# Optimization experiments

Measured on AMD Instinct MI355X. Metric: run time of the kernel, lower is better.

## Reference

```python
import jax, jax.numpy as jnp
import numpy as np

N_NODES = 50000
N_EDGES = 600000
D_EMB = 128
D_HID = 128
N_HEADS = 4
N_MABS = 7  # ISAB0(mab0,mab1), ISAB1(mab0,mab1), PMA, SAB, SAB
B, S = 16, 512
PROTO = 5


def setup_inputs() -> dict:
    key = jax.random.key(0)
    ks = jax.random.split(key, 24)
    nrm = lambda k, shape, s=0.05: jax.random.normal(k, shape, jnp.float32) * s
    node_embed = nrm(ks[0], (N_NODES + 1, D_EMB), 1.0).at[0].set(0.0)  # padding_idx=0
    return {
        'node_ids': jax.random.randint(ks[1], (B, S), 0, N_NODES),
        'edge_idx': jax.random.randint(ks[2], (2, N_EDGES), 0, N_NODES),
        'edge_attr': jax.random.normal(ks[3], (N_EDGES,), jnp.float32),
        'node_embed': node_embed,
        'lin_W': nrm(ks[4], (D_EMB, D_HID)), 'lin_b': jnp.zeros((D_HID,), jnp.float32),
        'gat_W': nrm(ks[5], (D_HID, D_HID)),
        'gat_att_src': nrm(ks[6], (D_HID,)), 'gat_att_dst': nrm(ks[7], (D_HID,)),
        'gat_bias': jnp.zeros((D_HID,), jnp.float32),
        'mab_Wq': nrm(ks[8], (N_MABS, D_HID, D_HID)), 'mab_bq': jnp.zeros((N_MABS, D_HID), jnp.float32),
        'mab_Wk': nrm(ks[9], (N_MABS, D_HID, D_HID)), 'mab_bk': jnp.zeros((N_MABS, D_HID), jnp.float32),
        'mab_Wv': nrm(ks[10], (N_MABS, D_HID, D_HID)), 'mab_bv': jnp.zeros((N_MABS, D_HID), jnp.float32),
        'mab_Wo': nrm(ks[11], (N_MABS, D_HID, D_HID)), 'mab_bo': jnp.zeros((N_MABS, D_HID), jnp.float32),
        'isab_I': nrm(ks[12], (2, 1, D_HID), 1.0),   # 2 ISAB blocks, num_inds=1
        'pma_S': nrm(ks[13], (1, D_HID), 1.0),       # num_outputs=1 seed
        'dec_W': nrm(ks[14], (D_HID, D_HID)), 'dec_b': jnp.zeros((D_HID,), jnp.float32),
        'prototypes': nrm(ks[15], (1, PROTO, D_HID), 1.0),
    }


def mab(Q, K, Wq, bq, Wk, bk, Wv, bv, Wo, bo):
    # Set-transformer MAB, ln=False; residual uses projected Q; scale by sqrt(full dim)
    D = Q.shape[-1]
    h, d = N_HEADS, D // N_HEADS
    Qp = Q @ Wq + bq
    Kp = K @ Wk + bk
    Vp = K @ Wv + bv
    sh = lambda x: x.reshape(x.shape[0], x.shape[1], h, d).transpose(0, 2, 1, 3)
    A = jax.nn.softmax(jnp.einsum('bhqd,bhkd->bhqk', sh(Qp), sh(Kp)) / np.sqrt(D).astype(np.float32))
    O = sh(Qp) + jnp.einsum('bhqk,bhkd->bhqd', A, sh(Vp))
    O = O.transpose(0, 2, 1, 3).reshape(Q.shape[0], Q.shape[1], D)
    return O + jax.nn.relu(O @ Wo + bo)


def reference(node_ids, edge_idx, edge_attr, node_embed, lin_W, lin_b, gat_W,
              gat_att_src, gat_att_dst, gat_bias, mab_Wq, mab_bq, mab_Wk, mab_bk,
              mab_Wv, mab_bv, mab_Wo, mab_bo, isab_I, pma_S, dec_W, dec_b, prototypes):
    # embed all nodes then linear
    x = node_embed[jnp.arange(N_NODES)] @ lin_W + lin_b          # [N, H]
    # GATConv (1 head, negative_slope=0.2, add_self_loops=True; edge_attr unused)
    loops = jnp.arange(N_NODES)
    src = jnp.concatenate([edge_idx[0], loops])
    dst = jnp.concatenate([edge_idx[1], loops])
    xw = x @ gat_W                                               # [N, H]
    a_s = xw @ gat_att_src                                       # [N]
    a_d = xw @ gat_att_dst
    e = jax.nn.leaky_relu(a_s[src] + a_d[dst], 0.2)              # [E+N]
    m = jax.ops.segment_max(e, dst, num_segments=N_NODES)
    ex = jnp.exp(e - m[dst])
    den = jax.ops.segment_sum(ex, dst, num_segments=N_NODES)
    coef = ex / den[dst]
    x = jax.ops.segment_sum(coef[:, None] * xw[src], dst, num_segments=N_NODES) + gat_bias
    # gather per-sample node sets
    X = x[node_ids]                                              # [B, S, H]
    b = X.shape[0]
    def mb(i, Q, K):
        return mab(Q, K, mab_Wq[i], mab_bq[i], mab_Wk[i], mab_bk[i],
                   mab_Wv[i], mab_bv[i], mab_Wo[i], mab_bo[i])
    # encoder: 2 ISAB blocks (num_inds=1)
    for i in range(2):
        Hb = mb(2 * i, jnp.broadcast_to(isab_I[i][None], (b, 1, D_HID)), X)
        X = mb(2 * i + 1, X, Hb)
    # decoder: PMA -> SAB -> SAB -> Linear
    X = mb(4, jnp.broadcast_to(pma_S[None], (b, 1, D_HID)), X)
    X = mb(5, X, X)
    X = mb(6, X, X)
    X = X @ dec_W + dec_b                                        # [B, 1, H]
    proto = jnp.broadcast_to(prototypes, (b, PROTO, D_HID))
    return jnp.concatenate([X, proto], axis=1)                   # [B, 6, H]
```

## Files before the change

kernel.cpp:

```cpp
#include <hip/hip_runtime.h>
#include <math.h>

#define N_NODES 50000
#define N_EDGES 600000
#define BATCH 16
#define SEQ 512
#define NROWS (BATCH*SEQ)
#define N_ITEMS (N_EDGES + N_NODES)

#define OFF_X      0L
#define OFF_ACC    1048576L
#define OFF_X2     2097152L
#define OFF_AS     3145728L
#define OFF_AD     3195728L
#define OFF_WC     3245728L
#define OFF_BC     3262112L
#define OFF_QP     3262240L
#define OFF_WKH    3262624L
#define OFF_CKH    3264160L
#define OFF_VAS    3264176L
#define OFF_VAD    3264304L
#define OFF_BFIN   3264432L
#define OFF_CSD    3264560L
#define OFF_VPOD   3264564L
#define OFF_UP     3266612L
#define OFF_SP     3332148L
#define OFF_PWH    3332660L
#define OFF_PWL    3373620L
#define OFF_MASK   3414580L
#define OFF_DEG    (OFF_MASK + 50000L)
#define OFF_FILL   (OFF_DEG + 8192L)
#define OFF_CNT    (OFF_FILL + 8192L)
#define ZERO_BYTES ((50000L + 8192L + 8192L + 4L) * 4L)
#define OFF_MAP    (OFF_CNT + 4L)
#define OFF_INV    (OFF_MAP + 50000L)
#define OFF_ROWPTR (OFF_INV + 8192L)
#define OFF_COL    (OFF_ROWPTR + 8194L)

typedef __attribute__((ext_vector_type(8))) short bf16x8;
typedef __attribute__((ext_vector_type(4))) float f32x4;
#define MFMA16(a,b,c) __builtin_amdgcn_mfma_f32_16x16x32_bf16(a,b,c,0,0,0)

__device__ __forceinline__ unsigned short f2bf_rne(float f) {
    unsigned int u = __float_as_uint(f);
    unsigned int r = u + 0x7FFFu + ((u >> 16) & 1u);
    return (unsigned short)(r >> 16);
}
__device__ __forceinline__ float bf2f(unsigned short h) {
    return __uint_as_float(((unsigned int)h) << 16);
}

__global__ __launch_bounds__(256) void prep_kernel(
    const float* __restrict__ lin_W, const float* __restrict__ lin_b,
    const float* __restrict__ gat_W,
    const float* __restrict__ mab_Wq, const float* __restrict__ mab_bq,
    const float* __restrict__ isab_I, const float* __restrict__ pma_S,
    float* __restrict__ Wc, float* __restrict__ bc, float* __restrict__ qp)
{
    int t = blockIdx.x * 256 + threadIdx.x;
    if (t < 16384) {
        int i = t >> 7, j = t & 127;
        float s = 0.f;
        for (int k = 0; k < 128; ++k) s += lin_W[i*128 + k] * gat_W[k*128 + j];
        Wc[t] = s;
    } else if (t < 16512) {
        int j = t - 16384;
        float s = 0.f;
        for (int k = 0; k < 128; ++k) s += lin_b[k] * gat_W[k*128 + j];
        bc[j] = s;
    } else if (t < 16896) {
        int u = t - 16512;
        int m = u >> 7, c = u & 127;
        int mi = m * 2;
        const float* vec = (m == 0) ? isab_I : (m == 1 ? isab_I + 128 : pma_S);
        float s = mab_bq[mi*128 + c];
        for (int k = 0; k < 128; ++k) s += vec[k] * mab_Wq[mi*16384 + k*128 + c];
        qp[u] = s;
    }
}

__global__ __launch_bounds__(256) void pack2_kernel(
    const float* __restrict__ Wc, const float* __restrict__ bc,
    const float* __restrict__ qp,
    const float* __restrict__ mab_Wq, const float* __restrict__ mab_Wo,
    const float* __restrict__ mab_Wk, const float* __restrict__ mab_bk,
    const float* __restrict__ att_src, const float* __restrict__ att_dst,
    const float* __restrict__ gat_bias,
    unsigned short* __restrict__ pWh, unsigned short* __restrict__ pWl,
    float* __restrict__ wkh, float* __restrict__ ckh,
    float* __restrict__ vas, float* __restrict__ vad,
    float* __restrict__ bfin, float* __restrict__ csd)
{
    int b = blockIdx.x, t = threadIdx.x;
    if (b < 320) {
        int tid = b*256 + t;
        int m = tid >> 14;
        int e = tid & 16383;
        int j = e & 7, l = (e>>3) & 63, ct = (e>>9) & 7, kc = e >> 12;
        int k = kc*32 + (l>>4)*8 + j;
        int c = ct*16 + (l & 15);
        const float* src;
        if (m == 0) src = Wc;
        else if (m == 1) src = mab_Wq + 1*16384;
        else if (m == 2) src = mab_Wo + 1*16384;
        else if (m == 3) src = mab_Wq + 3*16384;
        else src = mab_Wo + 3*16384;
        float v = src[k*128 + c];
        unsigned short h = f2bf_rne(v);
        pWh[tid] = h;
        pWl[tid] = f2bf_rne(v - bf2f(h));
    } else if (b == 320) {
        for (int it = 0; it < 6; ++it) {
            int u = it*256 + t;
            int m = u >> 9, h = (u >> 7) & 3, j = u & 127;
            const float* Wk = mab_Wk + (2*m)*16384 + j*128 + h*32;
            const float* q  = qp + m*128 + h*32;
            float s = 0.f;
            #pragma unroll
            for (int d = 0; d < 32; ++d) s += Wk[d] * q[d];
            wkh[u] = s;
        }
        if (t < 12) {
            int m = t >> 2, h = t & 3;
            const float* bk = mab_bk + (2*m)*128 + h*32;
            const float* q  = qp + m*128 + h*32;
            float s = 0.f;
            #pragma unroll
            for (int d = 0; d < 32; ++d) s += bk[d] * q[d];
            ckh[t] = s;
        }
    } else {
        if (t < 128) {
            float s = 0.f;
            for (int j = 0; j < 128; ++j) s += Wc[t*128 + j] * att_src[j];
            vas[t] = s;
            bfin[t] = bc[t] + gat_bias[t];
        } else {
            int k = t - 128;
            float s = 0.f;
            for (int j = 0; j < 128; ++j) s += Wc[k*128 + j] * att_dst[j];
            vad[k] = s;
        }
        if (t == 0) {
            float s = 0.f;
            for (int j = 0; j < 128; ++j) s += bc[j] * att_src[j];
            csd[0] = s;
        }
        if (t == 1) {
            float s = 0.f;
            for (int j = 0; j < 128; ++j) s += bc[j] * att_dst[j];
            csd[1] = s;
        }
    }
}

__device__ __forceinline__ void mfma_stage(
    const float (*Xs)[132], int arow, int ao, int lane,
    const unsigned short* __restrict__ pWh, const unsigned short* __restrict__ pWl,
    f32x4 acc[8])
{
    #pragma unroll
    for (int kc = 0; kc < 4; ++kc) {
        float4 fa = *(const float4*)&Xs[arow][kc*32 + ao];
        float4 fb = *(const float4*)&Xs[arow][kc*32 + ao + 4];
        float f[8] = {fa.x, fa.y, fa.z, fa.w, fb.x, fb.y, fb.z, fb.w};
        bf16x8 ah, al;
        #pragma unroll
        for (int j = 0; j < 8; ++j) {
            unsigned short h = f2bf_rne(f[j]);
            ah[j] = (short)h;
            al[j] = (short)f2bf_rne(f[j] - bf2f(h));
        }
        #pragma unroll
        for (int ct = 0; ct < 8; ++ct) {
            int fo = ((kc*8 + ct)*64 + lane)*8;
            bf16x8 bh = *(const bf16x8*)(pWh + fo);
            bf16x8 bl = *(const bf16x8*)(pWl + fo);
            acc[ct] = MFMA16(ah, bh, acc[ct]);
            acc[ct] = MFMA16(ah, bl, acc[ct]);
            acc[ct] = MFMA16(al, bh, acc[ct]);
        }
    }
}

__global__ __launch_bounds__(256) void mfma_lin_kernel(
    const float* __restrict__ Xin,
    const unsigned short* __restrict__ pWh, const unsigned short* __restrict__ pWl,
    const float* __restrict__ b1, float* __restrict__ out)
{
    __shared__ float Xs[64][132];
    int t = threadIdx.x;
    long row0 = (long)blockIdx.x * 64;
    #pragma unroll
    for (int i = 0; i < 32; ++i) {
        int idx = i*256 + t;
        int r = idx >> 7, k = idx & 127;
        Xs[r][k] = Xin[(row0 + r)*128 + k];
    }
    __syncthreads();
    int lane = t & 63, wv = t >> 6;
    int arow = wv*16 + (lane & 15), ao = (lane >> 4)*8;
    int crow0 = wv*16 + (lane >> 4)*4, ccol = lane & 15;
    f32x4 acc[8];
    #pragma unroll
    for (int ct = 0; ct < 8; ++ct) { acc[ct][0]=0.f; acc[ct][1]=0.f; acc[ct][2]=0.f; acc[ct][3]=0.f; }
    mfma_stage(Xs, arow, ao, lane, pWh, pWl, acc);
    #pragma unroll
    for (int ct = 0; ct < 8; ++ct) {
        int cc = ct*16 + ccol;
        float bb = b1[cc];
        #pragma unroll
        for (int i = 0; i < 4; ++i)
            out[(row0 + crow0 + i)*128 + cc] = acc[ct][i] + bb;
    }
}

__global__ __launch_bounds__(256) void mfma_odd_kernel(
    const float* __restrict__ Xin,
    const unsigned short* __restrict__ pQh, const unsigned short* __restrict__ pQl,
    const float* __restrict__ bq, const float* __restrict__ vpod,
    const unsigned short* __restrict__ pOh, const unsigned short* __restrict__ pOl,
    const float* __restrict__ bo, float* __restrict__ Xout)
{
    __shared__ float Xs[64][132];
    int t = threadIdx.x;
    long row0 = (long)blockIdx.x * 64;
    #pragma unroll
    for (int i = 0; i < 32; ++i) {
        int idx = i*256 + t;
        int r = idx >> 7, k = idx & 127;
        Xs[r][k] = Xin[(row0 + r)*128 + k];
    }
    __syncthreads();
    int lane = t & 63, wv = t >> 6;
    int arow = wv*16 + (lane & 15), ao = (lane >> 4)*8;
    int crow0 = wv*16 + (lane >> 4)*4, ccol = lane & 15;
    int bidx = (int)(row0 >> 9);
    f32x4 acc[8];
    #pragma unroll
    for (int ct = 0; ct < 8; ++ct) { acc[ct][0]=0.f; acc[ct][1]=0.f; acc[ct][2]=0.f; acc[ct][3]=0.f; }
    mfma_stage(Xs, arow, ao, lane, pQh, pQl, acc);
    #pragma unroll
    for (int ct = 0; ct < 8; ++ct) {
        int cc = ct*16 + ccol;
        float bb = bq[cc] + vpod[bidx*128 + cc];
        #pragma unroll
        for (int i = 0; i < 4; ++i) Xs[crow0 + i][cc] = acc[ct][i] + bb;
    }
    #pragma unroll
    for (int ct = 0; ct < 8; ++ct) { acc[ct][0]=0.f; acc[ct][1]=0.f; acc[ct][2]=0.f; acc[ct][3]=0.f; }
    mfma_stage(Xs, arow, ao, lane, pOh, pOl, acc);
    #pragma unroll
    for (int ct = 0; ct < 8; ++ct) {
        int cc = ct*16 + ccol;
        float bb = bo[cc];
        #pragma unroll
        for (int i = 0; i < 4; ++i) {
            float o1 = Xs[crow0 + i][cc];
            Xout[(row0 + crow0 + i)*128 + cc] = o1 + fmaxf(acc[ct][i] + bb, 0.f);
        }
    }
}

__global__ __launch_bounds__(256) void avec_kernel(
    const float* __restrict__ embed, const float* __restrict__ vas,
    const float* __restrict__ vad, const float* __restrict__ csd,
    const int* __restrict__ node_ids, int* __restrict__ mask,
    float* __restrict__ a_s, float* __restrict__ a_d)
{
    if (blockIdx.x < 32) {
        int idx = blockIdx.x*256 + threadIdx.x;
        mask[node_ids[idx]] = 1;
    }
    int w = threadIdx.x >> 6, lane = threadIdx.x & 63;
    long row = (long)blockIdx.x * 4 + w;
    const float* xr = embed + row*128 + lane*2;
    float x0 = xr[0], x1 = xr[1];
    float s = x0*vas[lane*2] + x1*vas[lane*2 + 1];
    float d = x0*vad[lane*2] + x1*vad[lane*2 + 1];
    #pragma unroll
    for (int off = 32; off > 0; off >>= 1) {
        s += __shfl_down(s, off);
        d += __shfl_down(d, off);
    }
    if (lane == 0) { a_s[row] = s + csd[0]; a_d[row] = d + csd[1]; }
}

__global__ __launch_bounds__(256) void assign_kernel(
    const int* __restrict__ mask, int* __restrict__ map,
    int* __restrict__ inv, int* __restrict__ counter)
{
    __shared__ int wbase[4];
    int i = blockIdx.x*256 + threadIdx.x;
    bool act = (i < N_NODES) && mask[i];
    unsigned long long m = __ballot(act);
    int lane = threadIdx.x & 63;
    int w = threadIdx.x >> 6;
    if (lane == 0) wbase[w] = __popcll(m);
    __syncthreads();
    if (threadIdx.x == 0) {
        int tot = wbase[0] + wbase[1] + wbase[2] + wbase[3];
        int base = atomicAdd(counter, tot);
        int r = base;
        #pragma unroll
        for (int j = 0; j < 4; ++j) { int cj = wbase[j]; wbase[j] = r; r += cj; }
    }
    __syncthreads();
    if (i < N_NODES) {
        int c = -1;
        if (act) {
            c = wbase[w] + __popcll(m & ((1ull << lane) - 1ull));
            inv[c] = i;
        }
        map[i] = c;
    }
}

__global__ __launch_bounds__(256) void pass1_kernel(
    const int* __restrict__ edge_idx, const int* __restrict__ map,
    int* __restrict__ deg)
{
    int i = blockIdx.x*256 + threadIdx.x;
    if (i >= N_ITEMS) return;
    int dd = (i < N_EDGES) ? edge_idx[N_EDGES + i] : i - N_EDGES;
    int c = map[dd];
    if (c >= 0) atomicAdd(&deg[c], 1);
}

__global__ __launch_bounds__(256) void scan_kernel(const int* __restrict__ deg,
                                                   int* __restrict__ rowptr)
{
    __shared__ int part[256];
    __shared__ int pref[256];
    int t = threadIdx.x;
    int base = t * 32;
    int s = 0;
    #pragma unroll
    for (int j = 0; j < 32; ++j) s += deg[base + j];
    part[t] = s;
    __syncthreads();
    if (t == 0) {
        int run = 0;
        for (int i = 0; i < 256; ++i) { pref[i] = run; run += part[i]; }
    }
    __syncthreads();
    int run = pref[t];
    #pragma unroll
    for (int j = 0; j < 32; ++j) { rowptr[base + j] = run; run += deg[base + j]; }
    if (t == 255) rowptr[8192] = run;
}

__global__ __launch_bounds__(256) void pass2_kernel(
    const int* __restrict__ edge_idx, const int* __restrict__ map,
    const int* __restrict__ rowptr, int* __restrict__ fill,
    int* __restrict__ colx)
{
    int i = blockIdx.x*256 + threadIdx.x;
    if (i >= N_ITEMS) return;
    int s, dd;
    if (i < N_EDGES) { s = edge_idx[i]; dd = edge_idx[N_EDGES + i]; }
    else             { s = dd = i - N_EDGES; }
    int c = map[dd];
    if (c < 0) return;
    int pos = rowptr[c] + atomicAdd(&fill[c], 1);
    colx[pos] = s;
}

__global__ __launch_bounds__(256) void agg_kernel(
    const int* __restrict__ rowptr, const int* __restrict__ colx,
    const int* __restrict__ inv, const int* __restrict__ cnt,
    const float* __restrict__ a_s, const float* __restrict__ a_d,
    const float* __restrict__ embed, float* __restrict__ acc)
{
    int c = blockIdx.x*4 + (threadIdx.x >> 6);
    int lane = threadIdx.x & 63;
    if (c >= *cnt) return;
    int dd = inv[c];
    float ad = a_d[dd];
    int beg = rowptr[c], end = rowptr[c + 1];
    float s0 = 0.f, s1 = 0.f, den = 0.f;
    for (int j = beg; j < end; ++j) {
        int s = colx[j];
        float e = a_s[s] + ad;
        e = (e > 0.f) ? e : 0.2f * e;
        float ex = __expf(e);
        den += ex;
        float2 v = *(const float2*)(embed + (long)s*128 + lane*2);
        s0 += ex * v.x;
        s1 += ex * v.y;
    }
    float inv_d = 1.f / den;
    float* o = acc + (long)c*128 + lane*2;
    o[0] = s0 * inv_d;
    o[1] = s1 * inv_d;
}

__global__ __launch_bounds__(256) void gather_kernel(
    const int* __restrict__ node_ids, const int* __restrict__ map,
    const float* __restrict__ X2, float* __restrict__ X)
{
    int w = threadIdx.x >> 6, lane = threadIdx.x & 63;
    int j = blockIdx.x*4 + w;
    int c = map[node_ids[j]];
    const float2 v = *(const float2*)(X2 + (long)c*128 + lane*2);
    *(float2*)(X + (long)j*128 + lane*2) = v;
}

__global__ __launch_bounds__(256) void attn_partA_kernel(
    const float* __restrict__ X, const float* __restrict__ wkh,
    const float* __restrict__ ckh, float* __restrict__ up, float* __restrict__ sp)
{
    __shared__ float wks[4][128];
    __shared__ float esm[4][64];
    int b = blockIdx.x >> 3, chunk = blockIdx.x & 7;
    int t = threadIdx.x;
    #pragma unroll
    for (int i = 0; i < 2; ++i) {
        int u = i*256 + t;
        wks[u >> 7][u & 127] = wkh[u];
    }
    __syncthreads();
    const float scale = 0.088388347648318447f;
    int wv = t >> 6, lane = t & 63;
    {
        const float* xr = X + ((long)b*512 + chunk*64 + lane)*128;
        float l = 0.f;
        for (int d4 = 0; d4 < 128; d4 += 4) {
            float4 xv = *(const float4*)&xr[d4];
            l += xv.x*wks[wv][d4] + xv.y*wks[wv][d4+1]
               + xv.z*wks[wv][d4+2] + xv.w*wks[wv][d4+3];
        }
        float e = __expf((l + ckh[wv]) * scale);
        esm[wv][lane] = e;
        float s = e;
        #pragma unroll
        for (int off = 32; off > 0; off >>= 1) s += __shfl_down(s, off);
        if (lane == 0) sp[(b*8 + chunk)*4 + wv] = s;
    }
    __syncthreads();
    {
        int hh = t >> 7, d = t & 127;
        float a0 = 0.f, a1 = 0.f;
        const float* xc = X + ((long)b*512 + chunk*64)*128 + d;
        for (int k = 0; k < 64; ++k) {
            float xv = xc[(long)k*128];
            a0 += esm[2*hh][k] * xv;
            a1 += esm[2*hh + 1][k] * xv;
        }
        up[((b*8 + chunk)*4 + 2*hh)*128 + d] = a0;
        up[((b*8 + chunk)*4 + 2*hh + 1)*128 + d] = a1;
    }
}

__device__ __forceinline__ float matvec_qs(
    const float* __restrict__ W, const float* xs, float (*red)[128], int t)
{
    int c = t & 127, q = t >> 7;
    float acc = 0.f;
    #pragma unroll
    for (int j = 0; j < 32; ++j) {
        int k = q*32 + j;
        acc += xs[k] * W[k*128 + c];
    }
    red[q][c] = acc;
    __syncthreads();
    float s = 0.f;
    if (t < 128) s = red[0][t] + red[1][t] + red[2][t] + red[3][t];
    __syncthreads();
    return s;
}

__global__ __launch_bounds__(512) void attn_evenB_kernel(
    const float* __restrict__ up, const float* __restrict__ sp,
    const float* __restrict__ qp,
    const float* __restrict__ Wv, const float* __restrict__ bv,
    const float* __restrict__ Wo, const float* __restrict__ bo,
    const float* __restrict__ Wv1, const float* __restrict__ bv1,
    float* __restrict__ vpod)
{
    __shared__ float u_sm[4][128];
    __shared__ float red[4][128];
    __shared__ float qs[128], Ovec[128], Hsm[128];
    int b = blockIdx.x, t = threadIdx.x;
    {
        float s = Wv[t*32] + Wo[t*32] + Wv1[t*32];
        asm volatile("" :: "v"(s));
    }
    if (t < 128) qs[t] = qp[t];
    {
        int h = t >> 7, d = t & 127;
        float s = 0.f, dn = 0.f;
        #pragma unroll
        for (int c = 0; c < 8; ++c) {
            s  += up[((b*8 + c)*4 + h)*128 + d];
            dn += sp[(b*8 + c)*4 + h];
        }
        u_sm[h][d] = s / dn;
    }
    __syncthreads();
    {
        int q4 = t >> 7, c = t & 127, h = c >> 5;
        float a = 0.f;
        #pragma unroll
        for (int j = 0; j < 32; ++j) {
            int k = q4*32 + j;
            a += u_sm[h][k] * Wv[k*128 + c];
        }
        red[q4][c] = a;
    }
    __syncthreads();
    if (t < 128) Ovec[t] = qs[t] + red[0][t] + red[1][t] + red[2][t] + red[3][t] + bv[t];
    __syncthreads();
    float mv = matvec_qs(Wo, Ovec, red, t);
    if (t < 128) Hsm[t] = Ovec[t] + fmaxf(mv + bo[t], 0.f);
    __syncthreads();
    float mv2 = matvec_qs(Wv1, Hsm, red, t);
    if (t < 128) vpod[b*128 + t] = mv2 + bv1[t];
}

__global__ __launch_bounds__(512) void attn_pmaB_kernel(
    const float* __restrict__ up, const float* __restrict__ sp,
    const float* __restrict__ qp,
    const float* __restrict__ mab_Wq, const float* __restrict__ mab_bq,
    const float* __restrict__ mab_Wv, const float* __restrict__ mab_bv,
    const float* __restrict__ mab_Wo, const float* __restrict__ mab_bo,
    const float* __restrict__ dec_W, const float* __restrict__ dec_b,
    const float* __restrict__ protos, float* __restrict__ out)
{
    __shared__ float u_sm[4][128];
    __shared__ float red[4][128];
    __shared__ float qs[128], Ovec[128], S1[128], S2[128];
    int b = blockIdx.x, t = threadIdx.x;
    {
        const float* wq = mab_Wq + 5*16384;
        const float* wv = mab_Wv + 4*16384;
        const float* wo = mab_Wo + 4*16384;
        float s = 0.f;
        #pragma unroll
        for (int i = 0; i < 2; ++i) s += wq[(t + 512*i)*32];
        #pragma unroll
        for (int i = 0; i < 3; ++i) { s += wv[(t + 512*i)*32]; s += wo[(t + 512*i)*32]; }
        s += dec_W[t*32];
        asm volatile("" :: "v"(s));
    }
    if (t < 128) qs[t] = qp[t];
    {
        int h = t >> 7, d = t & 127;
        float s = 0.f, dn = 0.f;
        #pragma unroll
        for (int c = 0; c < 8; ++c) {
            s  += up[((b*8 + c)*4 + h)*128 + d];
            dn += sp[(b*8 + c)*4 + h];
        }
        u_sm[h][d] = s / dn;
    }
    __syncthreads();
    {
        int q4 = t >> 7, c = t & 127, h = c >> 5;
        float a = 0.f;
        #pragma unroll
        for (int j = 0; j < 32; ++j) {
            int k = q4*32 + j;
            a += u_sm[h][k] * (mab_Wv + 4*16384)[k*128 + c];
        }
        red[q4][c] = a;
    }
    __syncthreads();
    if (t < 128) Ovec[t] = qs[t] + red[0][t] + red[1][t] + red[2][t] + red[3][t]
                         + mab_bv[4*128 + t];
    __syncthreads();
    float mv = matvec_qs(mab_Wo + 4*16384, Ovec, red, t);
    if (t < 128) S1[t] = Ovec[t] + fmaxf(mv + mab_bo[4*128 + t], 0.f);
    __syncthreads();
    float q5 = matvec_qs(mab_Wq + 5*16384, S1, red, t);
    float v5 = matvec_qs(mab_Wv + 5*16384, S1, red, t);
    if (t < 128) S2[t] = q5 + mab_bq[5*128 + t] + v5 + mab_bv[5*128 + t];
    __syncthreads();
    float m5 = matvec_qs(mab_Wo + 5*16384, S2, red, t);
    if (t < 128) S1[t] = S2[t] + fmaxf(m5 + mab_bo[5*128 + t], 0.f);
    __syncthreads();
    float q6 = matvec_qs(mab_Wq + 6*16384, S1, red, t);
    float v6 = matvec_qs(mab_Wv + 6*16384, S1, red, t);
    if (t < 128) S2[t] = q6 + mab_bq[6*128 + t] + v6 + mab_bv[6*128 + t];
    __syncthreads();
    float m6 = matvec_qs(mab_Wo + 6*16384, S2, red, t);
    if (t < 128) S1[t] = S2[t] + fmaxf(m6 + mab_bo[6*128 + t], 0.f);
    __syncthreads();
    float y = matvec_qs(dec_W, S1, red, t);
    if (t < 128) out[b*768 + t] = y + dec_b[t];
    {
        int p = t >> 7, c = t & 127;
        out[b*768 + (1 + p)*128 + c] = protos[p*128 + c];
        if (t < 128) out[b*768 + 640 + t] = protos[512 + t];
    }
}

extern "C" void kernel_launch(void* const* d_in, const int* in_sizes, int n_in,
                              void* d_out, int out_size, void* d_ws, size_t ws_size,
                              hipStream_t stream)
{
    (void)in_sizes; (void)n_in; (void)out_size; (void)ws_size;
    const int*   node_ids  = (const int*)d_in[0];
    const int*   edge_idx  = (const int*)d_in[1];
    const float* node_embed= (const float*)d_in[3];
    const float* lin_W     = (const float*)d_in[4];
    const float* lin_b     = (const float*)d_in[5];
    const float* gat_W     = (const float*)d_in[6];
    const float* att_src   = (const float*)d_in[7];
    const float* att_dst   = (const float*)d_in[8];
    const float* gat_bias  = (const float*)d_in[9];
    const float* mab_Wq    = (const float*)d_in[10];
    const float* mab_bq    = (const float*)d_in[11];
    const float* mab_Wk    = (const float*)d_in[12];
    const float* mab_bk    = (const float*)d_in[13];
    const float* mab_Wv    = (const float*)d_in[14];
    const float* mab_bv    = (const float*)d_in[15];
    const float* mab_Wo    = (const float*)d_in[16];
    const float* mab_bo    = (const float*)d_in[17];
    const float* isab_I    = (const float*)d_in[18];
    const float* pma_S     = (const float*)d_in[19];
    const float* dec_W     = (const float*)d_in[20];
    const float* dec_b     = (const float*)d_in[21];
    const float* protos    = (const float*)d_in[22];

    float* ws    = (float*)d_ws;
    float* X     = ws + OFF_X;
    float* acc   = ws + OFF_ACC;
    float* X2    = ws + OFF_X2;
    float* a_s   = ws + OFF_AS;
    float* a_d   = ws + OFF_AD;
    float* Wc    = ws + OFF_WC;
    float* bc    = ws + OFF_BC;
    float* qp    = ws + OFF_QP;
    float* wkh   = ws + OFF_WKH;
    float* ckh   = ws + OFF_CKH;
    float* vas   = ws + OFF_VAS;
    float* vad   = ws + OFF_VAD;
    float* bfin  = ws + OFF_BFIN;
    float* csd   = ws + OFF_CSD;
    float* vpod  = ws + OFF_VPOD;
    float* up    = ws + OFF_UP;
    float* sp    = ws + OFF_SP;
    unsigned short* pWh = (unsigned short*)(ws + OFF_PWH);
    unsigned short* pWl = (unsigned short*)(ws + OFF_PWL);
    int*   mask  = (int*)(ws + OFF_MASK);
    int*   deg   = (int*)(ws + OFF_DEG);
    int*   fill  = (int*)(ws + OFF_FILL);
    int*   cnt   = (int*)(ws + OFF_CNT);
    int*   map   = (int*)(ws + OFF_MAP);
    int*   inv   = (int*)(ws + OFF_INV);
    int*   rowp  = (int*)(ws + OFF_ROWPTR);
    int*   colx  = (int*)(ws + OFF_COL);
    float* out   = (float*)d_out;

    hipMemsetAsync(ws + OFF_MASK, 0, ZERO_BYTES, stream);

    prep_kernel<<<66, 256, 0, stream>>>(lin_W, lin_b, gat_W, mab_Wq, mab_bq, isab_I, pma_S,
                                        Wc, bc, qp);
    pack2_kernel<<<322, 256, 0, stream>>>(Wc, bc, qp, mab_Wq, mab_Wo, mab_Wk, mab_bk,
                                          att_src, att_dst, gat_bias,
                                          pWh, pWl, wkh, ckh, vas, vad, bfin, csd);
    avec_kernel<<<N_NODES/4, 256, 0, stream>>>(node_embed, vas, vad, csd, node_ids, mask,
                                               a_s, a_d);
    assign_kernel<<<(N_NODES + 255)/256, 256, 0, stream>>>(mask, map, inv, cnt);
    pass1_kernel<<<(N_ITEMS + 255)/256, 256, 0, stream>>>(edge_idx, map, deg);
    scan_kernel<<<1, 256, 0, stream>>>(deg, rowp);
    pass2_kernel<<<(N_ITEMS + 255)/256, 256, 0, stream>>>(edge_idx, map, rowp, fill, colx);
    agg_kernel<<<NROWS/4, 256, 0, stream>>>(rowp, colx, inv, cnt, a_s, a_d, node_embed, acc);
    mfma_lin_kernel<<<NROWS/64, 256, 0, stream>>>(acc, pWh, pWl, bfin, X2);
    gather_kernel<<<NROWS/4, 256, 0, stream>>>(node_ids, map, X2, X);

    for (int i = 0; i < 2; ++i) {
        int o = 2*i + 1;
        attn_partA_kernel<<<128, 256, 0, stream>>>(X, wkh + i*512, ckh + i*4, up, sp);
        attn_evenB_kernel<<<16, 512, 0, stream>>>(up, sp, qp + i*128,
                                                  mab_Wv + (2*i)*16384, mab_bv + (2*i)*128,
                                                  mab_Wo + (2*i)*16384, mab_bo + (2*i)*128,
                                                  mab_Wv + o*16384, mab_bv + o*128,
                                                  vpod);
        int mq = 1 + 2*i;
        int mo = 2 + 2*i;
        mfma_odd_kernel<<<NROWS/64, 256, 0, stream>>>(X,
                                                      pWh + mq*16384, pWl + mq*16384,
                                                      mab_bq + o*128, vpod,
                                                      pWh + mo*16384, pWl + mo*16384,
                                                      mab_bo + o*128, X);
    }
    attn_partA_kernel<<<128, 256, 0, stream>>>(X, wkh + 1024, ckh + 8, up, sp);
    attn_pmaB_kernel<<<16, 512, 0, stream>>>(up, sp, qp + 256,
                                             mab_Wq, mab_bq, mab_Wv, mab_bv, mab_Wo, mab_bo,
                                             dec_W, dec_b, protos, out);
}
```

Before: 279.1 us.

## Fuse attention partA into gather and odd MAB kernels, drop avec pass

Removes the avec kernel, which computed per-node attention scalars for all 50000 nodes, and instead computes source/destination scores on the fly inside agg_kernel with wave reductions over the embedding rows it already loads. The node mask setup moves into extra blocks of pack2. The gather and attn_partA kernels are fused into gatherA, and partA is also fused into the tail of the odd MAB kernel, reusing the shared-memory tile instead of rereading X from global memory. The scan is rewritten with a wave-level shuffle prefix in place of a serial loop. The trade-off is a redundant per-edge dot product and reduction in agg, plus fewer launches and less global traffic.

```diff
diff --git a/kernel.cpp b/kernel.cpp
--- a/kernel.cpp
+++ b/kernel.cpp
@@ -11,8 +11,6 @@
 #define OFF_X      0L
 #define OFF_ACC    1048576L
 #define OFF_X2     2097152L
-#define OFF_AS     3145728L
-#define OFF_AD     3195728L
 #define OFF_WC     3245728L
 #define OFF_BC     3262112L
 #define OFF_QP     3262240L
@@ -49,6 +47,11 @@
 __device__ __forceinline__ float bf2f(unsigned short h) {
     return __uint_as_float(((unsigned int)h) << 16);
 }
+__device__ __forceinline__ float wave_allsum(float x) {
+    #pragma unroll
+    for (int off = 32; off > 0; off >>= 1) x += __shfl_xor(x, off);
+    return x;
+}
 
 __global__ __launch_bounds__(256) void prep_kernel(
     const float* __restrict__ lin_W, const float* __restrict__ lin_b,
@@ -85,11 +88,12 @@
     const float* __restrict__ mab_Wq, const float* __restrict__ mab_Wo,
     const float* __restrict__ mab_Wk, const float* __restrict__ mab_bk,
     const float* __restrict__ att_src, const float* __restrict__ att_dst,
-    const float* __restrict__ gat_bias,
+    const float* __restrict__ gat_bias, const int* __restrict__ node_ids,
     unsigned short* __restrict__ pWh, unsigned short* __restrict__ pWl,
     float* __restrict__ wkh, float* __restrict__ ckh,
     float* __restrict__ vas, float* __restrict__ vad,
-    float* __restrict__ bfin, float* __restrict__ csd)
+    float* __restrict__ bfin, float* __restrict__ csd,
+    int* __restrict__ mask)
 {
     int b = blockIdx.x, t = threadIdx.x;
     if (b < 320) {
@@ -129,7 +133,7 @@
             for (int d = 0; d < 32; ++d) s += bk[d] * q[d];
             ckh[t] = s;
         }
-    } else {
+    } else if (b == 321) {
         if (t < 128) {
             float s = 0.f;
             for (int j = 0; j < 128; ++j) s += Wc[t*128 + j] * att_src[j];
@@ -151,6 +155,9 @@
             for (int j = 0; j < 128; ++j) s += bc[j] * att_dst[j];
             csd[1] = s;
         }
+    } else {
+        int idx = (b - 322)*256 + t;
+        mask[node_ids[idx]] = 1;
     }
 }
 
@@ -183,6 +190,41 @@
     }
 }
 
+__device__ __forceinline__ void partA_phase(
+    const float (*Xs)[132], const float (*wks)[128], float (*esm)[64],
+    const float* __restrict__ ckh, int blk, int t,
+    float* __restrict__ up, float* __restrict__ sp)
+{
+    const float scale = 0.088388347648318447f;
+    int wv = t >> 6, lane = t & 63;
+    {
+        float l = 0.f;
+        for (int d4 = 0; d4 < 128; d4 += 4) {
+            float4 xv = *(const float4*)&Xs[lane][d4];
+            l += xv.x*wks[wv][d4] + xv.y*wks[wv][d4+1]
+               + xv.z*wks[wv][d4+2] + xv.w*wks[wv][d4+3];
+        }
+        float e = __expf((l + ckh[wv]) * scale);
+        esm[wv][lane] = e;
+        float s = e;
+        #pragma unroll
+        for (int off = 32; off > 0; off >>= 1) s += __shfl_down(s, off);
+        if (lane == 0) sp[blk*4 + wv] = s;
+    }
+    __syncthreads();
+    {
+        int hh = t >> 7, d = t & 127;
+        float a0 = 0.f, a1 = 0.f;
+        for (int k = 0; k < 64; ++k) {
+            float xv = Xs[k][d];
+            a0 += esm[2*hh][k] * xv;
+            a1 += esm[2*hh + 1][k] * xv;
+        }
+        up[(blk*4 + 2*hh)*128 + d] = a0;
+        up[(blk*4 + 2*hh + 1)*128 + d] = a1;
+    }
+}
+
 __global__ __launch_bounds__(256) void mfma_lin_kernel(
     const float* __restrict__ Xin,
     const unsigned short* __restrict__ pWh, const unsigned short* __restrict__ pWl,
@@ -215,22 +257,56 @@
     }
 }
 
-__global__ __launch_bounds__(256) void mfma_odd_kernel(
+__global__ __launch_bounds__(256) void gatherA_kernel(
+    const int* __restrict__ node_ids, const int* __restrict__ map,
+    const float* __restrict__ X2, const float* __restrict__ wkh,
+    const float* __restrict__ ckh,
+    float* __restrict__ X, float* __restrict__ up, float* __restrict__ sp)
+{
+    __shared__ float Xs[64][132];
+    __shared__ float wks[4][128];
+    __shared__ float esm[4][64];
+    __shared__ int cmap[64];
+    int blk = blockIdx.x, t = threadIdx.x;
+    long j0 = (long)blk * 64;
+    if (t < 64) cmap[t] = map[node_ids[j0 + t]];
+    #pragma unroll
+    for (int i = 0; i < 2; ++i) { int u = i*256 + t; wks[u >> 7][u & 127] = wkh[u]; }
+    __syncthreads();
+    #pragma unroll
+    for (int i = 0; i < 8; ++i) {
+        int idx = i*256 + t;
+        int r = idx >> 5, k4 = (idx & 31)*4;
+        float4 v = *(const float4*)(X2 + (long)cmap[r]*128 + k4);
+        *(float4*)&Xs[r][k4] = v;
+        *(float4*)(X + (j0 + r)*128 + k4) = v;
+    }
+    __syncthreads();
+    partA_phase(Xs, wks, esm, ckh, blk, t, up, sp);
+}
+
+__global__ __launch_bounds__(256) void odd_fused_kernel(
     const float* __restrict__ Xin,
     const unsigned short* __restrict__ pQh, const unsigned short* __restrict__ pQl,
     const float* __restrict__ bq, const float* __restrict__ vpod,
     const unsigned short* __restrict__ pOh, const unsigned short* __restrict__ pOl,
-    const float* __restrict__ bo, float* __restrict__ Xout)
+    const float* __restrict__ bo,
+    const float* __restrict__ wkh, const float* __restrict__ ckh,
+    float* __restrict__ Xout, float* __restrict__ up, float* __restrict__ sp)
 {
     __shared__ float Xs[64][132];
-    int t = threadIdx.x;
-    long row0 = (long)blockIdx.x * 64;
+    __shared__ float wks[4][128];
+    __shared__ float esm[4][64];
+    int blk = blockIdx.x, t = threadIdx.x;
+    long row0 = (long)blk * 64;
     #pragma unroll
     for (int i = 0; i < 32; ++i) {
         int idx = i*256 + t;
         int r = idx >> 7, k = idx & 127;
         Xs[r][k] = Xin[(row0 + r)*128 + k];
     }
+    #pragma unroll
+    for (int i = 0; i < 2; ++i) { int u = i*256 + t; wks[u >> 7][u & 127] = wkh[u]; }
     __syncthreads();
     int lane = t & 63, wv = t >> 6;
     int arow = wv*16 + (lane & 15), ao = (lane >> 4)*8;
@@ -257,33 +333,13 @@
         #pragma unroll
         for (int i = 0; i < 4; ++i) {
             float o1 = Xs[crow0 + i][cc];
-            Xout[(row0 + crow0 + i)*128 + cc] = o1 + fmaxf(acc[ct][i] + bb, 0.f);
-        }
-    }
-}
-
-__global__ __launch_bounds__(256) void avec_kernel(
-    const float* __restrict__ embed, const float* __restrict__ vas,
-    const float* __restrict__ vad, const float* __restrict__ csd,
-    const int* __restrict__ node_ids, int* __restrict__ mask,
-    float* __restrict__ a_s, float* __restrict__ a_d)
-{
-    if (blockIdx.x < 32) {
-        int idx = blockIdx.x*256 + threadIdx.x;
-        mask[node_ids[idx]] = 1;
-    }
-    int w = threadIdx.x >> 6, lane = threadIdx.x & 63;
-    long row = (long)blockIdx.x * 4 + w;
-    const float* xr = embed + row*128 + lane*2;
-    float x0 = xr[0], x1 = xr[1];
-    float s = x0*vas[lane*2] + x1*vas[lane*2 + 1];
-    float d = x0*vad[lane*2] + x1*vad[lane*2 + 1];
-    #pragma unroll
-    for (int off = 32; off > 0; off >>= 1) {
-        s += __shfl_down(s, off);
-        d += __shfl_down(d, off);
-    }
-    if (lane == 0) { a_s[row] = s + csd[0]; a_d[row] = d + csd[1]; }
+            float v = o1 + fmaxf(acc[ct][i] + bb, 0.f);
+            Xout[(row0 + crow0 + i)*128 + cc] = v;
+            Xs[crow0 + i][cc] = v;
+        }
+    }
+    __syncthreads();
+    partA_phase(Xs, wks, esm, ckh, blk, t, up, sp);
 }
 
 __global__ __launch_bounds__(256) void assign_kernel(
@@ -330,21 +386,24 @@
 __global__ __launch_bounds__(256) void scan_kernel(const int* __restrict__ deg,
                                                    int* __restrict__ rowptr)
 {
-    __shared__ int part[256];
-    __shared__ int pref[256];
+    __shared__ int wsum[4];
     int t = threadIdx.x;
     int base = t * 32;
     int s = 0;
     #pragma unroll
     for (int j = 0; j < 32; ++j) s += deg[base + j];
-    part[t] = s;
-    __syncthreads();
-    if (t == 0) {
-        int run = 0;
-        for (int i = 0; i < 256; ++i) { pref[i] = run; run += part[i]; }
-    }
-    __syncthreads();
-    int run = pref[t];
+    int lane = t & 63, w = t >> 6;
+    int v = s;
+    #pragma unroll
+    for (int off = 1; off < 64; off <<= 1) {
+        int n = __shfl_up(v, off);
+        if (lane >= off) v += n;
+    }
+    if (lane == 63) wsum[w] = v;
+    __syncthreads();
+    int wo = 0;
+    for (int i = 0; i < 4; ++i) if (i < w) wo += wsum[i];
+    int run = wo + v - s;
     #pragma unroll
     for (int j = 0; j < 32; ++j) { rowptr[base + j] = run; run += deg[base + j]; }
     if (t == 255) rowptr[8192] = run;
@@ -369,23 +428,29 @@
 __global__ __launch_bounds__(256) void agg_kernel(
     const int* __restrict__ rowptr, const int* __restrict__ colx,
     const int* __restrict__ inv, const int* __restrict__ cnt,
-    const float* __restrict__ a_s, const float* __restrict__ a_d,
+    const float* __restrict__ vas, const float* __restrict__ vad,
+    const float* __restrict__ csd,
     const float* __restrict__ embed, float* __restrict__ acc)
 {
     int c = blockIdx.x*4 + (threadIdx.x >> 6);
     int lane = threadIdx.x & 63;
     if (c >= *cnt) return;
+    float va0 = vas[2*lane], va1 = vas[2*lane + 1];
+    float vb0 = vad[2*lane], vb1 = vad[2*lane + 1];
+    float csd0 = csd[0], csd1 = csd[1];
     int dd = inv[c];
-    float ad = a_d[dd];
+    float2 wrow = *(const float2*)(embed + (long)dd*128 + lane*2);
+    float ad = wave_allsum(wrow.x*vb0 + wrow.y*vb1) + csd1;
     int beg = rowptr[c], end = rowptr[c + 1];
     float s0 = 0.f, s1 = 0.f, den = 0.f;
     for (int j = beg; j < end; ++j) {
         int s = colx[j];
-        float e = a_s[s] + ad;
+        float2 v = *(const float2*)(embed + (long)s*128 + lane*2);
+        float as = wave_allsum(v.x*va0 + v.y*va1) + csd0;
+        float e = as + ad;
         e = (e > 0.f) ? e : 0.2f * e;
         float ex = __expf(e);
         den += ex;
-        float2 v = *(const float2*)(embed + (long)s*128 + lane*2);
         s0 += ex * v.x;
         s1 += ex * v.y;
     }
@@ -393,63 +458,6 @@
     float* o = acc + (long)c*128 + lane*2;
     o[0] = s0 * inv_d;
     o[1] = s1 * inv_d;
-}
-
-__global__ __launch_bounds__(256) void gather_kernel(
-    const int* __restrict__ node_ids, const int* __restrict__ map,
-    const float* __restrict__ X2, float* __restrict__ X)
-{
-    int w = threadIdx.x >> 6, lane = threadIdx.x & 63;
-    int j = blockIdx.x*4 + w;
-    int c = map[node_ids[j]];
-    const float2 v = *(const float2*)(X2 + (long)c*128 + lane*2);
-    *(float2*)(X + (long)j*128 + lane*2) = v;
-}
-
-__global__ __launch_bounds__(256) void attn_partA_kernel(
-    const float* __restrict__ X, const float* __restrict__ wkh,
-    const float* __restrict__ ckh, float* __restrict__ up, float* __restrict__ sp)
-{
-    __shared__ float wks[4][128];
-    __shared__ float esm[4][64];
-    int b = blockIdx.x >> 3, chunk = blockIdx.x & 7;
-    int t = threadIdx.x;
-    #pragma unroll
-    for (int i = 0; i < 2; ++i) {
-        int u = i*256 + t;
-        wks[u >> 7][u & 127] = wkh[u];
-    }
-    __syncthreads();
-    const float scale = 0.088388347648318447f;
-    int wv = t >> 6, lane = t & 63;
-    {
-        const float* xr = X + ((long)b*512 + chunk*64 + lane)*128;
-        float l = 0.f;
-        for (int d4 = 0; d4 < 128; d4 += 4) {
-            float4 xv = *(const float4*)&xr[d4];
-            l += xv.x*wks[wv][d4] + xv.y*wks[wv][d4+1]
-               + xv.z*wks[wv][d4+2] + xv.w*wks[wv][d4+3];
-        }
-        float e = __expf((l + ckh[wv]) * scale);
-        esm[wv][lane] = e;
-        float s = e;
-        #pragma unroll
-        for (int off = 32; off > 0; off >>= 1) s += __shfl_down(s, off);
-        if (lane == 0) sp[(b*8 + chunk)*4 + wv] = s;
-    }
-    __syncthreads();
-    {
-        int hh = t >> 7, d = t & 127;
-        float a0 = 0.f, a1 = 0.f;
-        const float* xc = X + ((long)b*512 + chunk*64)*128 + d;
-        for (int k = 0; k < 64; ++k) {
-            float xv = xc[(long)k*128];
-            a0 += esm[2*hh][k] * xv;
-            a1 += esm[2*hh + 1][k] * xv;
-        }
-        up[((b*8 + chunk)*4 + 2*hh)*128 + d] = a0;
-        up[((b*8 + chunk)*4 + 2*hh + 1)*128 + d] = a1;
-    }
 }
 
 __device__ __forceinline__ float matvec_qs(
@@ -627,8 +635,6 @@
     float* X     = ws + OFF_X;
     float* acc   = ws + OFF_ACC;
     float* X2    = ws + OFF_X2;
-    float* a_s   = ws + OFF_AS;
-    float* a_d   = ws + OFF_AD;
     float* Wc    = ws + OFF_WC;
     float* bc    = ws + OFF_BC;
     float* qp    = ws + OFF_QP;
@@ -657,22 +663,20 @@
 
     prep_kernel<<<66, 256, 0, stream>>>(lin_W, lin_b, gat_W, mab_Wq, mab_bq, isab_I, pma_S,
                                         Wc, bc, qp);
-    pack2_kernel<<<322, 256, 0, stream>>>(Wc, bc, qp, mab_Wq, mab_Wo, mab_Wk, mab_bk,
-                                          att_src, att_dst, gat_bias,
-                                          pWh, pWl, wkh, ckh, vas, vad, bfin, csd);
-    avec_kernel<<<N_NODES/4, 256, 0, stream>>>(node_embed, vas, vad, csd, node_ids, mask,
-                                               a_s, a_d);
+    pack2_kernel<<<354, 256, 0, stream>>>(Wc, bc, qp, mab_Wq, mab_Wo, mab_Wk, mab_bk,
+                                          att_src, att_dst, gat_bias, node_ids,
+                                          pWh, pWl, wkh, ckh, vas, vad, bfin, csd, mask);
     assign_kernel<<<(N_NODES + 255)/256, 256, 0, stream>>>(mask, map, inv, cnt);
     pass1_kernel<<<(N_ITEMS + 255)/256, 256, 0, stream>>>(edge_idx, map, deg);
     scan_kernel<<<1, 256, 0, stream>>>(deg, rowp);
     pass2_kernel<<<(N_ITEMS + 255)/256, 256, 0, stream>>>(edge_idx, map, rowp, fill, colx);
-    agg_kernel<<<NROWS/4, 256, 0, stream>>>(rowp, colx, inv, cnt, a_s, a_d, node_embed, acc);
+    agg_kernel<<<NROWS/4, 256, 0, stream>>>(rowp, colx, inv, cnt, vas, vad, csd,
+                                            node_embed, acc);
     mfma_lin_kernel<<<NROWS/64, 256, 0, stream>>>(acc, pWh, pWl, bfin, X2);
-    gather_kernel<<<NROWS/4, 256, 0, stream>>>(node_ids, map, X2, X);
+    gatherA_kernel<<<NROWS/64, 256, 0, stream>>>(node_ids, map, X2, wkh, ckh, X, up, sp);
 
     for (int i = 0; i < 2; ++i) {
         int o = 2*i + 1;
-        attn_partA_kernel<<<128, 256, 0, stream>>>(X, wkh + i*512, ckh + i*4, up, sp);
         attn_evenB_kernel<<<16, 512, 0, stream>>>(up, sp, qp + i*128,
                                                   mab_Wv + (2*i)*16384, mab_bv + (2*i)*128,
                                                   mab_Wo + (2*i)*16384, mab_bo + (2*i)*128,
@@ -680,13 +684,14 @@
                                                   vpod);
         int mq = 1 + 2*i;
         int mo = 2 + 2*i;
-        mfma_odd_kernel<<<NROWS/64, 256, 0, stream>>>(X,
-                                                      pWh + mq*16384, pWl + mq*16384,
-                                                      mab_bq + o*128, vpod,
-                                                      pWh + mo*16384, pWl + mo*16384,
-                                                      mab_bo + o*128, X);
-    }
-    attn_partA_kernel<<<128, 256, 0, stream>>>(X, wkh + 1024, ckh + 8, up, sp);
+        odd_fused_kernel<<<NROWS/64, 256, 0, stream>>>(X,
+                                                       pWh + mq*16384, pWl + mq*16384,
+                                                       mab_bq + o*128, vpod,
+                                                       pWh + mo*16384, pWl + mo*16384,
+                                                       mab_bo + o*128,
+                                                       wkh + (i + 1)*512, ckh + (i + 1)*4,
+                                                       X, up, sp);
+    }
     attn_pmaB_kernel<<<16, 512, 0, stream>>>(up, sp, qp + 256,
                                              mab_Wq, mab_bq, mab_Wv, mab_bv, mab_Wo, mab_bo,
                                              dec_W, dec_b, protos, out);
```

Result: faster. 259.9 us (-6.9%).
